# Performance work log

Hardware: AMD Instinct MI355X
Metric: run time of the kernel (lower is better)

The kernel has to match this reference:

```python
import jax, jax.numpy as jnp
import numpy as np
from jax import lax

EPS = 1e-5

def silu(x):
    return x * jax.nn.sigmoid(x)

def setup_inputs() -> dict:
    key = jax.random.key(0)
    ks = jax.random.split(key, 8)
    B, T, H, W = 8, 32, 128, 128
    x = jax.random.normal(ks[0], (B, 1, T, H, W), jnp.float32)
    w_spatial = jax.random.normal(ks[1], (3, 1, 3, 3), jnp.float32) * 0.3
    b_spatial = jax.random.normal(ks[2], (3,), jnp.float32) * 0.1
    w_temporal = jax.random.normal(ks[3], (3, 1, 7, 1), jnp.float32) * 0.3
    b_temporal = jax.random.normal(ks[4], (3,), jnp.float32) * 0.1
    sn_weight = jnp.ones((1, 3, 1, 1, 1), jnp.float32)
    sn_bias = jnp.zeros((1, 3, 1, 1, 1), jnp.float32)
    mean_weight = jnp.ones((3,), jnp.float32)
    var_weight = jnp.ones((3,), jnp.float32)
    w_kv_s = jax.random.normal(ks[5], (2, T), jnp.float32) * (1.0 / np.sqrt(T))
    w_kv_t = jax.random.normal(ks[6], (2, H * W), jnp.float32) * (1.0 / np.sqrt(H * W))
    return dict(x=x, w_spatial=w_spatial, b_spatial=b_spatial,
                w_temporal=w_temporal, b_temporal=b_temporal,
                sn_weight=sn_weight, sn_bias=sn_bias,
                mean_weight=mean_weight, var_weight=var_weight,
                w_kv_s=w_kv_s, w_kv_t=w_kv_t)

def reference(x, w_spatial, b_spatial, w_temporal, b_temporal,
              sn_weight, sn_bias, mean_weight, var_weight, w_kv_s, w_kv_t):
    b, _, t, h, w = x.shape
    C = 3
    # --- spatial cone: timeIsHidden -> Conv2d(1,3,3,pad=1) -> SiLU ---
    xs = x.transpose(0, 2, 1, 3, 4).reshape(b * t, 1, h, w)  # (b t) c h w
    y = lax.conv_general_dilated(xs, w_spatial, (1, 1), ((1, 1), (1, 1)))
    y = silu(y + b_spatial[None, :, None, None])
    y = y.reshape(b, t, C, h, w).transpose(0, 2, 1, 3, 4)  # [b,3,t,h,w]
    # --- temporal cone: spaceIsHidden -> depthwise Conv2d(3,3,(7,1),groups=3) -> SiLU ---
    # kernel is (7,1) so convolving [b,3,t,hw] along t with width-1 in hw is identical math
    yt = y.reshape(b, C, t, h * w)
    z = lax.conv_general_dilated(yt, w_temporal, (1, 1), ((3, 3), (0, 0)),
                                 feature_group_count=C)
    z = silu(z + b_temporal[None, :, None, None]).reshape(b, C, t, h, w)
    # --- gain stage 1: SiLU + SwitchNorm3d(3) (training-mode statistics) ---
    g = silu(z)
    xr = g.reshape(b, C, -1)
    mean_in = xr.mean(-1, keepdims=True)              # [b,C,1] instance stats
    var_in = xr.var(-1, ddof=1, keepdims=True)        # torch .var is unbiased
    temp = var_in + mean_in ** 2
    mean_ln = mean_in.mean(1, keepdims=True)          # layer stats
    var_ln = temp.mean(1, keepdims=True) - mean_ln ** 2
    mean_bn = mean_in.mean(0, keepdims=True)          # batch stats
    var_bn = temp.mean(0, keepdims=True) - mean_bn ** 2
    mw = jax.nn.softmax(mean_weight)
    vw = jax.nn.softmax(var_weight)
    mean = mw[0] * mean_in + mw[1] * mean_ln + mw[2] * mean_bn
    var = vw[0] * var_in + vw[1] * var_ln + vw[2] * var_bn
    xn = ((xr - mean) / jnp.sqrt(var + EPS)).reshape(b, C, t, h, w)
    xn = xn * sn_weight + sn_bias
    # --- gain stage 2: GainControl (spatial/temporal kv via 1x1 convs) ---
    hw = h * w
    # to_kv_spatial: Conv2d(t,2,1,bias=False) over time-as-channel == contraction over t
    kv_s = jnp.einsum('bcthw,ot->bcohw', xn, w_kv_s)   # [b,C,2,h,w]
    ks_ = jax.nn.softmax(kv_s[:, :, 0].reshape(b, C, hw), axis=-1)[:, :, None, :]
    vs_ = kv_s[:, :, 1].reshape(b, C, hw)[:, :, None, :]
    # to_kv_temporal: Conv2d(hw,2,1,bias=False) over space-as-channel == contraction over hw
    xflat = xn.reshape(b, C, t, hw)
    kv_t = jnp.einsum('bcts,os->bcot', xflat, w_kv_t)  # [b,C,2,t]
    kt_ = jax.nn.softmax(kv_t[:, :, 0], axis=-1)[..., None]
    vt_ = kv_t[:, :, 1][..., None]
    out = jnp.sqrt(kt_ * ks_) * (vt_ * vs_)            # [b,C,t,hw]
    return out.reshape(b, C, t, h, w)
```

## Files before the change

### kernel.cpp

```cpp
#include <hip/hip_runtime.h>
#include <hip/hip_bf16.h>
#include <hip/hip_fp16.h>

#define Bn 8
#define Cn 3
#define Tn 32
#define Hn 128
#define Wn 128
#define HWn (Hn * Wn)
#define Nn (Tn * HWn)
#define EPSn 1e-5f
#define QT 4
#define SCH 128
#define SSW (SCH * QT)

__device__ __forceinline__ float silu_f(float v) {
    return v * __builtin_amdgcn_rcpf(1.0f + __expf(-v));
}

__global__ __launch_bounds__(256) void k1_spatial(
    const float* __restrict__ x, const float* __restrict__ wsp,
    const float* __restrict__ bsp, __half* __restrict__ y)
{
    const int tid = threadIdx.x;
    const int sub = tid & 31;
    const int bt = blockIdx.x;
    const int b = bt >> 5, t = bt & 31;
    const int row = blockIdx.y * 8 + (tid >> 5);
    const int col = sub * 4;

    float w[27], bb[3];
#pragma unroll
    for (int i = 0; i < 27; ++i) w[i] = wsp[i];
#pragma unroll
    for (int i = 0; i < 3; ++i) bb[i] = bsp[i];

    const float* xsl = x + ((size_t)b * Tn + t) * HWn + (size_t)row * Wn + col;
    const bool upok = row > 0, dnok = row < Hn - 1;
    const float4 z4 = make_float4(0.f, 0.f, 0.f, 0.f);
    float4 xm = upok ? *(const float4*)(xsl - Wn) : z4;
    float4 xc = *(const float4*)(xsl);
    float4 xp = dnok ? *(const float4*)(xsl + Wn) : z4;
    float xv[3][6];
    {
        float lu, rd;
        lu = __shfl_up(xm.w, 1);  rd = __shfl_down(xm.x, 1);
        xv[0][0] = (sub == 0) ? 0.f : lu; xv[0][1] = xm.x; xv[0][2] = xm.y;
        xv[0][3] = xm.z; xv[0][4] = xm.w; xv[0][5] = (sub == 31) ? 0.f : rd;
        lu = __shfl_up(xc.w, 1);  rd = __shfl_down(xc.x, 1);
        xv[1][0] = (sub == 0) ? 0.f : lu; xv[1][1] = xc.x; xv[1][2] = xc.y;
        xv[1][3] = xc.z; xv[1][4] = xc.w; xv[1][5] = (sub == 31) ? 0.f : rd;
        lu = __shfl_up(xp.w, 1);  rd = __shfl_down(xp.x, 1);
        xv[2][0] = (sub == 0) ? 0.f : lu; xv[2][1] = xp.x; xv[2][2] = xp.y;
        xv[2][3] = xp.z; xv[2][4] = xp.w; xv[2][5] = (sub == 31) ? 0.f : rd;
    }
#pragma unroll
    for (int c = 0; c < 3; ++c) {
        float s0 = bb[c], s1 = bb[c], s2 = bb[c], s3 = bb[c];
#pragma unroll
        for (int i = 0; i < 3; ++i) {
#pragma unroll
            for (int j = 0; j < 3; ++j) {
                const float wv = w[c * 9 + i * 3 + j];
                s0 += wv * xv[i][j];
                s1 += wv * xv[i][j + 1];
                s2 += wv * xv[i][j + 2];
                s3 += wv * xv[i][j + 3];
            }
        }
        __half2 o01 = __floats2half2_rn(silu_f(s0), silu_f(s1));
        __half2 o23 = __floats2half2_rn(silu_f(s2), silu_f(s3));
        __half2* dst = (__half2*)(y + ((size_t)(b * 3 + c) * Tn + t) * HWn
                                  + (size_t)row * Wn + col);
        dst[0] = o01; dst[1] = o23;
    }
}

template<int QTg>
__device__ __forceinline__ void k2_body(
    const __half* __restrict__ y, const float* __restrict__ wtp,
    const float* __restrict__ btp, const float* __restrict__ wkt,
    const float* __restrict__ wks,
    float* __restrict__ raw0, float* __restrict__ raw1,
    float* __restrict__ pt0p, float* __restrict__ pt1p,
    float* __restrict__ ss0p, float* __restrict__ ss1p)
{
    constexpr int O0 = QTg * 8;
    constexpr int O1 = O0 + 8;
    constexpr int SLO = (O0 - 3 < 0) ? 0 : (O0 - 3);
    constexpr int SHI = (O1 + 2 > Tn - 1) ? (Tn - 1) : (O1 + 2);

    const int tid = threadIdx.x, lane = tid & 63, wave = tid >> 6;
    const int sch = blockIdx.x * 4 + wave;
    const int bc  = blockIdx.y;
    const int c = bc % 3;
    const int s0i = sch * 128 + lane * 2;

    float wt_r[7];
#pragma unroll
    for (int i = 0; i < 7; ++i) wt_r[i] = wtp[c * 7 + i];
    const float bt_r = btp[c];

    const __half* yb = y + (size_t)bc * Nn + s0i;
    const float2 k0v = *(const float2*)(wkt + s0i);
    const float2 k1v = *(const float2*)(wkt + HWn + s0i);

    float2 ring[7];
    float2 a0 = make_float2(0.f, 0.f), a1 = make_float2(0.f, 0.f);
    float ps = 0.f, pq = 0.f;
    float pt0a[8], pt1a[8];

#pragma unroll
    for (int tt = SLO; tt <= SHI + 3; ++tt) {
        if (tt <= SHI) {
            const __half2 hv = *(const __half2*)(yb + (size_t)tt * HWn);
            ring[tt % 7] = __half22float2(hv);
        }
        const int to = tt - 3;
        if (to >= O0 && to < O1) {
            float t0 = bt_r, t1 = bt_r;
#pragma unroll
            for (int k = 0; k < 7; ++k) {
                const int ts = to + k - 3;
                if (ts >= 0 && ts < Tn) {
                    const float wv = wt_r[k];
                    t0 += wv * ring[ts % 7].x;
                    t1 += wv * ring[ts % 7].y;
                }
            }
            const float g0 = silu_f(silu_f(t0));
            const float g1 = silu_f(silu_f(t1));
            const float wk0 = wks[to];
            const float wk1 = wks[Tn + to];
            a0.x += wk0 * g0; a0.y += wk0 * g1;
            a1.x += wk1 * g0; a1.y += wk1 * g1;
            ps += g0 + g1;
            pq += g0 * g0 + g1 * g1;
            pt0a[to - O0] = k0v.x * g0 + k0v.y * g1;
            pt1a[to - O0] = k1v.x * g0 + k1v.y * g1;
        }
    }

#pragma unroll
    for (int i = 0; i < 8; ++i) {
        pt0a[i] += __shfl_xor(pt0a[i], 1, 64);
        pt0a[i] += __shfl_xor(pt0a[i], 2, 64);
        pt0a[i] += __shfl_xor(pt0a[i], 4, 64);
        pt1a[i] += __shfl_xor(pt1a[i], 1, 64);
        pt1a[i] += __shfl_xor(pt1a[i], 2, 64);
        pt1a[i] += __shfl_xor(pt1a[i], 4, 64);
    }
    {
        const int j = lane & 7;
        float r0 = (j == 0) ? pt0a[0] : (j == 1) ? pt0a[1] : (j == 2) ? pt0a[2]
                 : (j == 3) ? pt0a[3] : (j == 4) ? pt0a[4] : (j == 5) ? pt0a[5]
                 : (j == 6) ? pt0a[6] : pt0a[7];
        float r1 = (j == 0) ? pt1a[0] : (j == 1) ? pt1a[1] : (j == 2) ? pt1a[2]
                 : (j == 3) ? pt1a[3] : (j == 4) ? pt1a[4] : (j == 5) ? pt1a[5]
                 : (j == 6) ? pt1a[6] : pt1a[7];
        r0 += __shfl_xor(r0, 8, 64); r0 += __shfl_xor(r0, 16, 64); r0 += __shfl_xor(r0, 32, 64);
        r1 += __shfl_xor(r1, 8, 64); r1 += __shfl_xor(r1, 16, 64); r1 += __shfl_xor(r1, 32, 64);
        if (lane < 8)
            pt0p[((size_t)bc * Tn + O0 + lane) * SCH + sch] = r0;
        else if (lane < 16)
            pt1p[((size_t)bc * Tn + O0 + (lane & 7)) * SCH + sch] = r1;
    }
    {
        float p0 = ps, p1 = pq;
        p0 += __shfl_xor(p0, 1, 64); p0 += __shfl_xor(p0, 2, 64); p0 += __shfl_xor(p0, 4, 64);
        p1 += __shfl_xor(p1, 1, 64); p1 += __shfl_xor(p1, 2, 64); p1 += __shfl_xor(p1, 4, 64);
        float r = (lane & 1) ? p1 : p0;
        r += __shfl_xor(r, 8, 64);
        r += __shfl_xor(r, 16, 64);
        r += __shfl_xor(r, 32, 64);
        if (lane == 0) ss0p[(size_t)bc * SSW + sch * QT + QTg] = r;
        if (lane == 1) ss1p[(size_t)bc * SSW + sch * QT + QTg] = r;
    }
    {
        const size_t off = (size_t)(QTg * 24 + bc) * HWn + s0i;
        *(float2*)(raw0 + off) = a0;
        *(float2*)(raw1 + off) = a1;
    }
}

__global__ __launch_bounds__(256) void k2_temporal(
    const __half* __restrict__ y, const float* __restrict__ wtp,
    const float* __restrict__ btp, const float* __restrict__ wkt,
    const float* __restrict__ wks,
    float* __restrict__ raw0, float* __restrict__ raw1,
    float* __restrict__ pt0p, float* __restrict__ pt1p,
    float* __restrict__ ss0p, float* __restrict__ ss1p)
{
    switch (blockIdx.z) {
    case 0: k2_body<0>(y, wtp, btp, wkt, wks, raw0, raw1, pt0p, pt1p, ss0p, ss1p); break;
    case 1: k2_body<1>(y, wtp, btp, wkt, wks, raw0, raw1, pt0p, pt1p, ss0p, ss1p); break;
    case 2: k2_body<2>(y, wtp, btp, wkt, wks, raw0, raw1, pt0p, pt1p, ss0p, ss1p); break;
    default: k2_body<3>(y, wtp, btp, wkt, wks, raw0, raw1, pt0p, pt1p, ss0p, ss1p); break;
    }
}

__global__ __launch_bounds__(256) void k3a_reduce(
    const float* __restrict__ pt0p, const float* __restrict__ pt1p,
    const float* __restrict__ ss0p, const float* __restrict__ ss1p,
    const float* __restrict__ wkt, const float* __restrict__ wks,
    const float* __restrict__ raw0, const float* __restrict__ raw1,
    float* __restrict__ kvt0r, float* __restrict__ kvt1r,
    float* __restrict__ ssS, float* __restrict__ ssSS, float* __restrict__ wsum,
    float* __restrict__ v0s, float* __restrict__ v1s)
{
    const int blk = blockIdx.x;
    const int tid = threadIdx.x;
    if (blk < Bn * Cn) {
        const int t = tid >> 3, g = tid & 7;
        const float4* p0 = (const float4*)(pt0p + ((size_t)blk * Tn + t) * SCH) + g * 4;
        const float4* p1 = (const float4*)(pt1p + ((size_t)blk * Tn + t) * SCH) + g * 4;
        float4 A0 = p0[0], A1 = p0[1], A2 = p0[2], A3 = p0[3];
        float4 B0 = p1[0], B1 = p1[1], B2 = p1[2], B3 = p1[3];
        float s0 = ((A0.x + A0.y) + (A0.z + A0.w)) + ((A1.x + A1.y) + (A1.z + A1.w))
                 + ((A2.x + A2.y) + (A2.z + A2.w)) + ((A3.x + A3.y) + (A3.z + A3.w));
        float s1 = ((B0.x + B0.y) + (B0.z + B0.w)) + ((B1.x + B1.y) + (B1.z + B1.w))
                 + ((B2.x + B2.y) + (B2.z + B2.w)) + ((B3.x + B3.y) + (B3.z + B3.w));
        s0 += __shfl_xor(s0, 1, 64); s0 += __shfl_xor(s0, 2, 64); s0 += __shfl_xor(s0, 4, 64);
        s1 += __shfl_xor(s1, 1, 64); s1 += __shfl_xor(s1, 2, 64); s1 += __shfl_xor(s1, 4, 64);
        if (g == 0) { kvt0r[blk * Tn + t] = s0; kvt1r[blk * Tn + t] = s1; }
        const float4* q0 = (const float4*)(ss0p + (size_t)blk * SSW);
        const float4* q1 = (const float4*)(ss1p + (size_t)blk * SSW);
        float a = 0.f, bb = 0.f;
        if (tid < SSW / 4) {
            float4 a4 = q0[tid], b4 = q1[tid];
            a = (a4.x + a4.y) + (a4.z + a4.w);
            bb = (b4.x + b4.y) + (b4.z + b4.w);
        }
        __shared__ float r0[256], r1[256];
        r0[tid] = a; r1[tid] = bb;
        __syncthreads();
        for (int off = 128; off > 0; off >>= 1) {
            if (tid < off) { r0[tid] += r0[tid + off]; r1[tid] += r1[tid + off]; }
            __syncthreads();
        }
        if (tid == 0) { ssS[blk] = r0[0]; ssSS[blk] = r1[0]; }
    } else if (blk == Bn * Cn) {
        const float4* w0 = (const float4*)wkt;
        const float4* w1 = (const float4*)(wkt + HWn);
        float l0 = 0.f, l1 = 0.f;
        for (int i = tid; i < HWn / 4; i += 256) {
            float4 t0 = w0[i], t1 = w1[i];
            l0 += (t0.x + t0.y) + (t0.z + t0.w);
            l1 += (t1.x + t1.y) + (t1.z + t1.w);
        }
        __shared__ float r0[256], r1[256];
        r0[tid] = l0; r1[tid] = l1;
        __syncthreads();
        for (int off = 128; off > 0; off >>= 1) {
            if (tid < off) { r0[tid] += r0[tid + off]; r1[tid] += r1[tid + off]; }
            __syncthreads();
        }
        if (tid == 0) { wsum[0] = r0[0]; wsum[1] = r1[0]; }
        if (tid < 64) {
            float v = wks[tid];
            v += __shfl_xor(v, 1, 64); v += __shfl_xor(v, 2, 64);
            v += __shfl_xor(v, 4, 64); v += __shfl_xor(v, 8, 64);
            v += __shfl_xor(v, 16, 64);
            if (tid == 0) wsum[2] = v;
            if (tid == 32) wsum[3] = v;
        }
    } else {
        const int rs = blk - (Bn * Cn + 1);
        const int bc = rs >> 3, sl = rs & 7;
        const size_t idx = (size_t)bc * HWn + sl * 2048 + tid * 8;
        float4 a0 = make_float4(0.f, 0.f, 0.f, 0.f), a1 = a0, b0 = a0, b1 = a0;
#pragma unroll
        for (int q = 0; q < QT; ++q) {
            const float* p0 = raw0 + (size_t)q * 24 * HWn + idx;
            const float* p1 = raw1 + (size_t)q * 24 * HWn + idx;
            float4 t0 = ((const float4*)p0)[0], t1 = ((const float4*)p0)[1];
            float4 u0 = ((const float4*)p1)[0], u1 = ((const float4*)p1)[1];
            a0.x += t0.x; a0.y += t0.y; a0.z += t0.z; a0.w += t0.w;
            a1.x += t1.x; a1.y += t1.y; a1.z += t1.z; a1.w += t1.w;
            b0.x += u0.x; b0.y += u0.y; b0.z += u0.z; b0.w += u0.w;
            b1.x += u1.x; b1.y += u1.y; b1.z += u1.z; b1.w += u1.w;
        }
        ((float4*)(v0s + idx))[0] = a0; ((float4*)(v0s + idx))[1] = a1;
        ((float4*)(v1s + idx))[0] = b0; ((float4*)(v1s + idx))[1] = b1;
    }
}

__global__ __launch_bounds__(256) void k6_fused(
    const float* __restrict__ v0s, const float* __restrict__ v1s,
    const float* __restrict__ kvt0r, const float* __restrict__ kvt1r,
    const float* __restrict__ ssS, const float* __restrict__ ssSS,
    const float* __restrict__ wsum, const float* __restrict__ mean_w,
    const float* __restrict__ var_w, const float* __restrict__ snw,
    const float* __restrict__ snb, float* __restrict__ out)
{
    const int ch = blockIdx.x;
    const int bc = blockIdx.y;
    const int tid = threadIdx.x, lane = tid & 63, wave = tid >> 6;
    const int b = bc / 3, c = bc % 3;
    const float Nf = (float)Nn;

    float mln = 0.f, tln = 0.f;
#pragma unroll
    for (int cc = 0; cc < 3; ++cc) {
        float S = ssS[b * 3 + cc], SS = ssSS[b * 3 + cc];
        float m = S / Nf;
        float v = (SS - S * m) / (Nf - 1.0f);
        mln += m; tln += v + m * m;
    }
    mln *= (1.0f / 3.0f); tln *= (1.0f / 3.0f);
    const float vln = tln - mln * mln;
    float mbn = 0.f, tbn = 0.f;
#pragma unroll
    for (int bb2 = 0; bb2 < 8; ++bb2) {
        float S = ssS[bb2 * 3 + c], SS = ssSS[bb2 * 3 + c];
        float m = S / Nf;
        float v = (SS - S * m) / (Nf - 1.0f);
        mbn += m; tbn += v + m * m;
    }
    mbn *= 0.125f; tbn *= 0.125f;
    const float vbn = tbn - mbn * mbn;
    const float S_own = ssS[bc], SS_own = ssSS[bc];
    const float mean_in = S_own / Nf;
    const float var_in = (SS_own - S_own * mean_in) / (Nf - 1.0f);
    float mw0, mw1, mw2, vw0, vw1, vw2;
    {
        float m0 = mean_w[0], m1 = mean_w[1], m2 = mean_w[2];
        float mm = fmaxf(m0, fmaxf(m1, m2));
        float e0 = __expf(m0 - mm), e1 = __expf(m1 - mm), e2 = __expf(m2 - mm);
        float inv = 1.0f / (e0 + e1 + e2);
        mw0 = e0 * inv; mw1 = e1 * inv; mw2 = e2 * inv;
    }
    {
        float v0 = var_w[0], v1 = var_w[1], v2 = var_w[2];
        float vm = fmaxf(v0, fmaxf(v1, v2));
        float e0 = __expf(v0 - vm), e1 = __expf(v1 - vm), e2 = __expf(v2 - vm);
        float inv = 1.0f / (e0 + e1 + e2);
        vw0 = e0 * inv; vw1 = e1 * inv; vw2 = e2 * inv;
    }
    const float mean = mw0 * mean_in + mw1 * mln + mw2 * mbn;
    const float var  = vw0 * var_in + vw1 * vln + vw2 * vbn;
    const float sc = snw[c] / sqrtf(var + EPSn);
    const float sf = snb[c] - mean * sc;
    const float c0 = sf * wsum[2], c1 = sf * wsum[3];
    const float Wt0 = wsum[0], Wt1 = wsum[1];

    __shared__ float aSh[Tn];
    if (tid < Tn) {
        float k0 = sc * kvt0r[bc * Tn + tid] + sf * Wt0;
        float k1 = sc * kvt1r[bc * Tn + tid] + sf * Wt1;
        float m = k0;
#pragma unroll
        for (int d = 1; d < 32; d <<= 1) m = fmaxf(m, __shfl_xor(m, d, 64));
        float e = __expf(k0 - m);
        float s = e;
#pragma unroll
        for (int d = 1; d < 32; d <<= 1) s += __shfl_xor(s, d, 64);
        aSh[tid] = sqrtf(e / s) * k1;
    }

    const float* p0a = v0s + (size_t)bc * HWn;
    float mloc = -3.4e38f;
#pragma unroll
    for (int i = 0; i < 16; ++i) {
        const int idx = tid * 4 + i * 1024;
        float4 u = *(const float4*)(p0a + idx);
        mloc = fmaxf(mloc, fmaxf(fmaxf(sc * u.x + c0, sc * u.y + c0),
                                 fmaxf(sc * u.z + c0, sc * u.w + c0)));
    }
#pragma unroll
    for (int d = 1; d < 64; d <<= 1) mloc = fmaxf(mloc, __shfl_xor(mloc, d, 64));
    __shared__ float wred[4];
    if (lane == 0) wred[wave] = mloc;
    __syncthreads();
    const float M = fmaxf(fmaxf(wred[0], wred[1]), fmaxf(wred[2], wred[3]));
    __syncthreads();
    float sloc = 0.f;
#pragma unroll
    for (int i = 0; i < 16; ++i) {
        const int idx = tid * 4 + i * 1024;
        float4 u = *(const float4*)(p0a + idx);
        sloc += __expf(sc * u.x + c0 - M) + __expf(sc * u.y + c0 - M)
              + __expf(sc * u.z + c0 - M) + __expf(sc * u.w + c0 - M);
    }
#pragma unroll
    for (int d = 1; d < 64; d <<= 1) sloc += __shfl_xor(sloc, d, 64);
    if (lane == 0) wred[wave] = sloc;
    __syncthreads();
    const float Sexp = (wred[0] + wred[1]) + (wred[2] + wred[3]);
    const float invS = __builtin_amdgcn_rcpf(Sexp);

    const int s = ch * 1024 + tid * 4;
    float4 u0 = *(const float4*)(p0a + s);
    float4 u1 = *(const float4*)(v1s + (size_t)bc * HWn + s);
    float4 Bv;
    Bv.x = sqrtf(__expf(sc * u0.x + c0 - M) * invS) * (sc * u1.x + c1);
    Bv.y = sqrtf(__expf(sc * u0.y + c0 - M) * invS) * (sc * u1.y + c1);
    Bv.z = sqrtf(__expf(sc * u0.z + c0 - M) * invS) * (sc * u1.z + c1);
    Bv.w = sqrtf(__expf(sc * u0.w + c0 - M) * invS) * (sc * u1.w + c1);
    float* op = out + (size_t)bc * Nn + s;
#pragma unroll
    for (int t = 0; t < Tn; ++t) {
        const float av = aSh[t];
        float4 o; o.x = av * Bv.x; o.y = av * Bv.y; o.z = av * Bv.z; o.w = av * Bv.w;
        *(float4*)(op + (size_t)t * HWn) = o;
    }
}

extern "C" void kernel_launch(void* const* d_in, const int* in_sizes, int n_in,
                              void* d_out, int out_size, void* d_ws, size_t ws_size,
                              hipStream_t stream) {
    const float* x          = (const float*)d_in[0];
    const float* w_spatial  = (const float*)d_in[1];
    const float* b_spatial  = (const float*)d_in[2];
    const float* w_temporal = (const float*)d_in[3];
    const float* b_temporal = (const float*)d_in[4];
    const float* sn_weight  = (const float*)d_in[5];
    const float* sn_bias    = (const float*)d_in[6];
    const float* mean_weight= (const float*)d_in[7];
    const float* var_weight = (const float*)d_in[8];
    const float* w_kv_s     = (const float*)d_in[9];
    const float* w_kv_t     = (const float*)d_in[10];
    float* out = (float*)d_out;
    float* ws  = (float*)d_ws;

    __half* yh   = (__half*)ws;
    float* raw0  = ws + 6291456;
    float* raw1  = raw0 + (size_t)QT * Bn * Cn * HWn;
    float* pt0p  = raw1 + (size_t)QT * Bn * Cn * HWn;
    float* pt1p  = pt0p + (size_t)Bn * Cn * Tn * SCH;
    float* ss0p  = pt1p + (size_t)Bn * Cn * Tn * SCH;
    float* ss1p  = ss0p + (size_t)Bn * Cn * SSW;
    float* v0s   = ss1p + (size_t)Bn * Cn * SSW;
    float* v1s   = v0s + (size_t)Bn * Cn * HWn;
    float* kvt0r = v1s + (size_t)Bn * Cn * HWn;
    float* kvt1r = kvt0r + Bn * Cn * Tn;
    float* ssS   = kvt1r + Bn * Cn * Tn;
    float* ssSS  = ssS + 24;
    float* wsum  = ssSS + 24;

    k1_spatial<<<dim3(Bn * Tn, Hn / 8), 256, 0, stream>>>(x, w_spatial, b_spatial, yh);
    k2_temporal<<<dim3(SCH / 4, Bn * Cn, QT), 256, 0, stream>>>(yh, w_temporal,
                                                                b_temporal, w_kv_t,
                                                                w_kv_s, raw0, raw1,
                                                                pt0p, pt1p, ss0p, ss1p);
    k3a_reduce<<<Bn * Cn + 1 + 192, 256, 0, stream>>>(pt0p, pt1p, ss0p, ss1p,
                                                      w_kv_t, w_kv_s, raw0, raw1,
                                                      kvt0r, kvt1r, ssS, ssSS, wsum,
                                                      v0s, v1s);
    k6_fused<<<dim3(16, Bn * Cn), 256, 0, stream>>>(v0s, v1s, kvt0r, kvt1r,
                                                    ssS, ssSS, wsum, mean_weight,
                                                    var_weight, sn_weight, sn_bias, out);
}
```

Baseline: 55.44 us.

## Store intermediate partial-sum buffers in fp16 and use one-pass online softmax

The raw per-quarter partial sums and the reduced v0s/v1s spatial buffers change from fp32 to fp16, which halves their traffic through workspace memory. In k6, the two-pass max-then-sum softmax over v0s becomes a single online pass that tracks a running max and sum and merges them across lanes and waves, so the buffer is read once instead of twice. Workspace offsets are recomputed for the smaller buffers. The cost is fp16 rounding error on intermediates that feed exp and the output, plus extra exp calls in the online merge.

```diff
diff --git a/kernel.cpp b/kernel.cpp
--- a/kernel.cpp
+++ b/kernel.cpp
@@ -81,7 +81,7 @@
     const __half* __restrict__ y, const float* __restrict__ wtp,
     const float* __restrict__ btp, const float* __restrict__ wkt,
     const float* __restrict__ wks,
-    float* __restrict__ raw0, float* __restrict__ raw1,
+    __half* __restrict__ raw0, __half* __restrict__ raw1,
     float* __restrict__ pt0p, float* __restrict__ pt1p,
     float* __restrict__ ss0p, float* __restrict__ ss1p)
 {
@@ -178,8 +178,8 @@
     }
     {
         const size_t off = (size_t)(QTg * 24 + bc) * HWn + s0i;
-        *(float2*)(raw0 + off) = a0;
-        *(float2*)(raw1 + off) = a1;
+        *(__half2*)(raw0 + off) = __floats2half2_rn(a0.x, a0.y);
+        *(__half2*)(raw1 + off) = __floats2half2_rn(a1.x, a1.y);
     }
 }
 
@@ -187,7 +187,7 @@
     const __half* __restrict__ y, const float* __restrict__ wtp,
     const float* __restrict__ btp, const float* __restrict__ wkt,
     const float* __restrict__ wks,
-    float* __restrict__ raw0, float* __restrict__ raw1,
+    __half* __restrict__ raw0, __half* __restrict__ raw1,
     float* __restrict__ pt0p, float* __restrict__ pt1p,
     float* __restrict__ ss0p, float* __restrict__ ss1p)
 {
@@ -203,10 +203,10 @@
     const float* __restrict__ pt0p, const float* __restrict__ pt1p,
     const float* __restrict__ ss0p, const float* __restrict__ ss1p,
     const float* __restrict__ wkt, const float* __restrict__ wks,
-    const float* __restrict__ raw0, const float* __restrict__ raw1,
+    const __half* __restrict__ raw0, const __half* __restrict__ raw1,
     float* __restrict__ kvt0r, float* __restrict__ kvt1r,
     float* __restrict__ ssS, float* __restrict__ ssSS, float* __restrict__ wsum,
-    float* __restrict__ v0s, float* __restrict__ v1s)
+    __half* __restrict__ v0s, __half* __restrict__ v1s)
 {
     const int blk = blockIdx.x;
     const int tid = threadIdx.x;
@@ -268,25 +268,35 @@
         const int rs = blk - (Bn * Cn + 1);
         const int bc = rs >> 3, sl = rs & 7;
         const size_t idx = (size_t)bc * HWn + sl * 2048 + tid * 8;
-        float4 a0 = make_float4(0.f, 0.f, 0.f, 0.f), a1 = a0, b0 = a0, b1 = a0;
+        float acc0[8] = {0,0,0,0,0,0,0,0}, acc1[8] = {0,0,0,0,0,0,0,0};
 #pragma unroll
         for (int q = 0; q < QT; ++q) {
-            const float* p0 = raw0 + (size_t)q * 24 * HWn + idx;
-            const float* p1 = raw1 + (size_t)q * 24 * HWn + idx;
-            float4 t0 = ((const float4*)p0)[0], t1 = ((const float4*)p0)[1];
-            float4 u0 = ((const float4*)p1)[0], u1 = ((const float4*)p1)[1];
-            a0.x += t0.x; a0.y += t0.y; a0.z += t0.z; a0.w += t0.w;
-            a1.x += t1.x; a1.y += t1.y; a1.z += t1.z; a1.w += t1.w;
-            b0.x += u0.x; b0.y += u0.y; b0.z += u0.z; b0.w += u0.w;
-            b1.x += u1.x; b1.y += u1.y; b1.z += u1.z; b1.w += u1.w;
-        }
-        ((float4*)(v0s + idx))[0] = a0; ((float4*)(v0s + idx))[1] = a1;
-        ((float4*)(v1s + idx))[0] = b0; ((float4*)(v1s + idx))[1] = b1;
+            float4 h0 = *(const float4*)(raw0 + (size_t)q * 24 * HWn + idx);
+            float4 h1 = *(const float4*)(raw1 + (size_t)q * 24 * HWn + idx);
+            const __half2* p0 = (const __half2*)&h0;
+            const __half2* p1 = (const __half2*)&h1;
+#pragma unroll
+            for (int j = 0; j < 4; ++j) {
+                float2 f0 = __half22float2(p0[j]);
+                float2 f1 = __half22float2(p1[j]);
+                acc0[j * 2] += f0.x; acc0[j * 2 + 1] += f0.y;
+                acc1[j * 2] += f1.x; acc1[j * 2 + 1] += f1.y;
+            }
+        }
+        float4 o0, o1;
+        __half2* s0 = (__half2*)&o0; __half2* s1 = (__half2*)&o1;
+#pragma unroll
+        for (int j = 0; j < 4; ++j) {
+            s0[j] = __floats2half2_rn(acc0[j * 2], acc0[j * 2 + 1]);
+            s1[j] = __floats2half2_rn(acc1[j * 2], acc1[j * 2 + 1]);
+        }
+        *(float4*)(v0s + idx) = o0;
+        *(float4*)(v1s + idx) = o1;
     }
 }
 
 __global__ __launch_bounds__(256) void k6_fused(
-    const float* __restrict__ v0s, const float* __restrict__ v1s,
+    const __half* __restrict__ v0s, const __half* __restrict__ v1s,
     const float* __restrict__ kvt0r, const float* __restrict__ kvt1r,
     const float* __restrict__ ssS, const float* __restrict__ ssSS,
     const float* __restrict__ wsum, const float* __restrict__ mean_w,
@@ -358,45 +368,58 @@
         aSh[tid] = sqrtf(e / s) * k1;
     }
 
-    const float* p0a = v0s + (size_t)bc * HWn;
-    float mloc = -3.4e38f;
-#pragma unroll
-    for (int i = 0; i < 16; ++i) {
-        const int idx = tid * 4 + i * 1024;
-        float4 u = *(const float4*)(p0a + idx);
-        mloc = fmaxf(mloc, fmaxf(fmaxf(sc * u.x + c0, sc * u.y + c0),
-                                 fmaxf(sc * u.z + c0, sc * u.w + c0)));
-    }
-#pragma unroll
-    for (int d = 1; d < 64; d <<= 1) mloc = fmaxf(mloc, __shfl_xor(mloc, d, 64));
-    __shared__ float wred[4];
-    if (lane == 0) wred[wave] = mloc;
+    const __half* p0a = v0s + (size_t)bc * HWn;
+    float m_run = -3.4e38f, s_run = 0.f;
+#pragma unroll
+    for (int i = 0; i < 8; ++i) {
+        const int idx = tid * 8 + i * 2048;
+        float4 hv = *(const float4*)(p0a + idx);
+        const __half2* hp = (const __half2*)&hv;
+        float vals[8];
+#pragma unroll
+        for (int j = 0; j < 4; ++j) {
+            float2 f = __half22float2(hp[j]);
+            vals[j * 2] = sc * f.x + c0;
+            vals[j * 2 + 1] = sc * f.y + c0;
+        }
+        float vm = vals[0];
+#pragma unroll
+        for (int j = 1; j < 8; ++j) vm = fmaxf(vm, vals[j]);
+        const float mn = fmaxf(m_run, vm);
+        float sl = 0.f;
+#pragma unroll
+        for (int j = 0; j < 8; ++j) sl += __expf(vals[j] - mn);
+        s_run = s_run * __expf(m_run - mn) + sl;
+        m_run = mn;
+    }
+#pragma unroll
+    for (int d = 1; d < 64; d <<= 1) {
+        const float mo = __shfl_xor(m_run, d, 64);
+        const float so = __shfl_xor(s_run, d, 64);
+        const float mn = fmaxf(m_run, mo);
+        s_run = s_run * __expf(m_run - mn) + so * __expf(mo - mn);
+        m_run = mn;
+    }
+    __shared__ float wm[4], wsv[4];
+    if (lane == 0) { wm[wave] = m_run; wsv[wave] = s_run; }
     __syncthreads();
-    const float M = fmaxf(fmaxf(wred[0], wred[1]), fmaxf(wred[2], wred[3]));
-    __syncthreads();
-    float sloc = 0.f;
-#pragma unroll
-    for (int i = 0; i < 16; ++i) {
-        const int idx = tid * 4 + i * 1024;
-        float4 u = *(const float4*)(p0a + idx);
-        sloc += __expf(sc * u.x + c0 - M) + __expf(sc * u.y + c0 - M)
-              + __expf(sc * u.z + c0 - M) + __expf(sc * u.w + c0 - M);
-    }
-#pragma unroll
-    for (int d = 1; d < 64; d <<= 1) sloc += __shfl_xor(sloc, d, 64);
-    if (lane == 0) wred[wave] = sloc;
-    __syncthreads();
-    const float Sexp = (wred[0] + wred[1]) + (wred[2] + wred[3]);
+    float M = fmaxf(fmaxf(wm[0], wm[1]), fmaxf(wm[2], wm[3]));
+    float Sexp = wsv[0] * __expf(wm[0] - M) + wsv[1] * __expf(wm[1] - M)
+               + wsv[2] * __expf(wm[2] - M) + wsv[3] * __expf(wm[3] - M);
     const float invS = __builtin_amdgcn_rcpf(Sexp);
 
     const int s = ch * 1024 + tid * 4;
-    float4 u0 = *(const float4*)(p0a + s);
-    float4 u1 = *(const float4*)(v1s + (size_t)bc * HWn + s);
+    float2 h0 = *(const float2*)(p0a + s);
+    float2 h1 = *(const float2*)(v1s + (size_t)bc * HWn + s);
+    const __half2* q0 = (const __half2*)&h0;
+    const __half2* q1 = (const __half2*)&h1;
+    float2 u0l = __half22float2(q0[0]), u0h = __half22float2(q0[1]);
+    float2 u1l = __half22float2(q1[0]), u1h = __half22float2(q1[1]);
     float4 Bv;
-    Bv.x = sqrtf(__expf(sc * u0.x + c0 - M) * invS) * (sc * u1.x + c1);
-    Bv.y = sqrtf(__expf(sc * u0.y + c0 - M) * invS) * (sc * u1.y + c1);
-    Bv.z = sqrtf(__expf(sc * u0.z + c0 - M) * invS) * (sc * u1.z + c1);
-    Bv.w = sqrtf(__expf(sc * u0.w + c0 - M) * invS) * (sc * u1.w + c1);
+    Bv.x = sqrtf(__expf(sc * u0l.x + c0 - M) * invS) * (sc * u1l.x + c1);
+    Bv.y = sqrtf(__expf(sc * u0l.y + c0 - M) * invS) * (sc * u1l.y + c1);
+    Bv.z = sqrtf(__expf(sc * u0h.x + c0 - M) * invS) * (sc * u1h.x + c1);
+    Bv.w = sqrtf(__expf(sc * u0h.y + c0 - M) * invS) * (sc * u1h.y + c1);
     float* op = out + (size_t)bc * Nn + s;
 #pragma unroll
     for (int t = 0; t < Tn; ++t) {
@@ -424,15 +447,15 @@
     float* ws  = (float*)d_ws;
 
     __half* yh   = (__half*)ws;
-    float* raw0  = ws + 6291456;
-    float* raw1  = raw0 + (size_t)QT * Bn * Cn * HWn;
-    float* pt0p  = raw1 + (size_t)QT * Bn * Cn * HWn;
+    __half* raw0 = (__half*)(ws + 6291456);
+    __half* raw1 = raw0 + (size_t)QT * Bn * Cn * HWn;
+    float* pt0p  = ws + 6291456 + 2 * 786432;
     float* pt1p  = pt0p + (size_t)Bn * Cn * Tn * SCH;
     float* ss0p  = pt1p + (size_t)Bn * Cn * Tn * SCH;
     float* ss1p  = ss0p + (size_t)Bn * Cn * SSW;
-    float* v0s   = ss1p + (size_t)Bn * Cn * SSW;
-    float* v1s   = v0s + (size_t)Bn * Cn * HWn;
-    float* kvt0r = v1s + (size_t)Bn * Cn * HWn;
+    __half* v0s  = (__half*)(ss1p + (size_t)Bn * Cn * SSW);
+    __half* v1s  = v0s + (size_t)Bn * Cn * HWn;
+    float* kvt0r = (float*)(v1s + (size_t)Bn * Cn * HWn);
     float* kvt1r = kvt0r + Bn * Cn * Tn;
     float* ssS   = kvt1r + Bn * Cn * Tn;
     float* ssSS  = ssS + 24;
```

Measured after the change: 54.26 us (median of 2 runs). -2.1%, faster.
